# Optimization experiments

Measured on AMD Instinct MI355X. Metric: run time of the kernel, lower is better.

## Reference

```python
import jax, jax.numpy as jnp
import numpy as np

N = 100000
E = 3200000
NEG_SLOPE = 0.2  # PyG GATConv default


def gat_layer(x, src, dst, W, a_src, a_dst, b, heads, out_ch, concat):
    # per-node linear transform, split into heads: [N, H, C]
    h = (x @ W).reshape(N, heads, out_ch)
    # per-node attention logits: [N, H]
    al_src = jnp.sum(h * a_src, axis=-1)
    al_dst = jnp.sum(h * a_dst, axis=-1)
    # per-edge attention coefficient (x_j = source, x_i = target): [E, H]
    e = jax.nn.leaky_relu(al_src[src] + al_dst[dst], NEG_SLOPE)
    # segment softmax over incoming edges of each destination node
    m = jax.ops.segment_max(e, dst, num_segments=N)
    e = jnp.exp(e - m[dst])
    denom = jax.ops.segment_sum(e, dst, num_segments=N)
    alpha = e / (denom[dst] + 1e-16)
    # weighted message aggregation: scatter-add over dst
    msg = h[src] * alpha[..., None]  # [E, H, C]
    out = jax.ops.segment_sum(msg, dst, num_segments=N)  # [N, H, C]
    out = out.reshape(N, heads * out_ch) if concat else out.mean(axis=1)
    return out + b


def setup_inputs() -> dict:
    key = jax.random.key(0)
    ks = jax.random.split(key, 11)
    return {
        "x": jax.random.normal(ks[0], (N, 2), dtype=jnp.float32),
        "edge_index": jax.random.randint(ks[1], (2, E), 0, N, dtype=jnp.int64),
        "edge_attr": jax.random.normal(ks[2], (E, 1), dtype=jnp.float32),
        "W1": jax.random.normal(ks[3], (2, 32), dtype=jnp.float32) * 0.5,
        "att_src1": jax.random.normal(ks[4], (4, 8), dtype=jnp.float32) * 0.3,
        "att_dst1": jax.random.normal(ks[5], (4, 8), dtype=jnp.float32) * 0.3,
        "b1": jnp.zeros((32,), dtype=jnp.float32),
        "W2": jax.random.normal(ks[6], (32, 2), dtype=jnp.float32) * 0.2,
        "att_src2": jax.random.normal(ks[7], (1, 2), dtype=jnp.float32) * 0.3,
        "att_dst2": jax.random.normal(ks[8], (1, 2), dtype=jnp.float32) * 0.3,
        "b2": jnp.zeros((2,), dtype=jnp.float32),
    }


def reference(x, edge_index, edge_attr, W1, att_src1, att_dst1, b1, W2, att_src2, att_dst2, b2):
    # add self-loops (PyG GATConv default add_self_loops=True)
    loops = jnp.arange(N, dtype=edge_index.dtype)
    src = jnp.concatenate([edge_index[0], loops])
    dst = jnp.concatenate([edge_index[1], loops])
    h = gat_layer(x, src, dst, W1, att_src1, att_dst1, b1, heads=4, out_ch=8, concat=True)
    h = jax.nn.elu(h)
    out = gat_layer(h, src, dst, W2, att_src2, att_dst2, b2, heads=1, out_ch=2, concat=False)
    return out
```

## Files before the change

kernel.cpp:

```cpp
#include <hip/hip_runtime.h>
#include <math.h>

#define NEG_SLOPE 0.2f
#define BK_BITS 8
#define BK (1 << BK_BITS)
#define SBITS 17
#define SMASK ((1 << SBITS) - 1)
#define CAP 9216
#define CELL 80
#define NSLOT (256 * CELL)
#define RNDS 20
#define SW(p) ((p) ^ (((p) >> 5) & 31))

__device__ __forceinline__ float lrelu(float x) { return x > 0.f ? x : NEG_SLOPE * x; }

__global__ __launch_bounds__(1024) void bucket_scatter(const int* __restrict__ src,
                                                       const int* __restrict__ dst,
                                                       int* __restrict__ cnt_g,
                                                       int* __restrict__ cells, int E) {
    __shared__ int cnt[512], off[512], cur[512];
    __shared__ int2 lpair[12504];
    __shared__ int sTot;
    int t = threadIdx.x;
    int blk = blockIdx.x;
    int nb = gridDim.x;
    if (t < 512) cnt[t] = 0;
    __syncthreads();

    int E4 = E >> 2;
    int chunk4 = (E4 + nb - 1) / nb;
    const int4* src4 = (const int4*)src;
    const int4* dst4 = (const int4*)dst;
    int base4 = blk * chunk4;
    int4 d4[4], s4[4];
    bool val[4];
#pragma unroll
    for (int k = 0; k < 4; k++) {
        int o = k * 1024 + t;
        int i4 = base4 + o;
        val[k] = (o < chunk4) && (i4 < E4);
        if (val[k]) { d4[k] = dst4[i4]; s4[k] = src4[i4]; }
    }
    int dt = -1, st = 0;
    if (blk == nb - 1) {
        int e = (E4 << 2) + t;
        if (e < E) { dt = dst[e]; st = src[e]; }
    }
#pragma unroll
    for (int k = 0; k < 4; k++) {
        if (val[k]) {
            atomicAdd(&cnt[d4[k].x >> BK_BITS], 1);
            atomicAdd(&cnt[d4[k].y >> BK_BITS], 1);
            atomicAdd(&cnt[d4[k].z >> BK_BITS], 1);
            atomicAdd(&cnt[d4[k].w >> BK_BITS], 1);
        }
    }
    if (dt >= 0) atomicAdd(&cnt[dt >> BK_BITS], 1);
    __syncthreads();

    if (t < 512) cnt_g[blk * 512 + t] = min(cnt[t], CELL);
    if (t < 64) {
        int v[8], mysum = 0;
#pragma unroll
        for (int k = 0; k < 8; k++) { v[k] = cnt[t * 8 + k]; mysum += v[k]; }
        int s = mysum;
#pragma unroll
        for (int o = 1; o < 64; o <<= 1) {
            int u = __shfl_up(s, o);
            if (t >= o) s += u;
        }
        int run = s - mysum;
#pragma unroll
        for (int k = 0; k < 8; k++) {
            int d2 = t * 8 + k;
            off[d2] = run; cur[d2] = run;
            run += v[k];
        }
        if (t == 63) sTot = s;
    }
    __syncthreads();
    int total = sTot;

#pragma unroll
    for (int k = 0; k < 4; k++) {
        if (val[k]) {
            int slot;
            slot = atomicAdd(&cur[d4[k].x >> BK_BITS], 1); lpair[slot] = make_int2(d4[k].x, s4[k].x);
            slot = atomicAdd(&cur[d4[k].y >> BK_BITS], 1); lpair[slot] = make_int2(d4[k].y, s4[k].y);
            slot = atomicAdd(&cur[d4[k].z >> BK_BITS], 1); lpair[slot] = make_int2(d4[k].z, s4[k].z);
            slot = atomicAdd(&cur[d4[k].w >> BK_BITS], 1); lpair[slot] = make_int2(d4[k].w, s4[k].w);
        }
    }
    if (dt >= 0) {
        int slot = atomicAdd(&cur[dt >> BK_BITS], 1);
        lpair[slot] = make_int2(dt, st);
    }
    __syncthreads();

    int cellbase = blk * CELL;
    for (int i = t; i < total; i += 1024) {
        int2 e = lpair[i];
        int b = e.x >> BK_BITS;
        int slot = i - off[b];
        if (slot < CELL)
            cells[(size_t)b * NSLOT + cellbase + slot] =
                ((e.x & (BK - 1)) << SBITS) | e.y;
    }
}

__global__ __launch_bounds__(1024) void agg1_sortgather(
        const int* __restrict__ cells, const int* __restrict__ cnt_g,
        const float2* __restrict__ x2,
        const float* __restrict__ W1, const float* __restrict__ asrc,
        const float* __restrict__ adst, const float* __restrict__ b1,
        const float* __restrict__ W2, const float* __restrict__ as2,
        const float* __restrict__ ad2,
        float2* __restrict__ h2, float* __restrict__ al2d,
        int* __restrict__ rowdeg, int* __restrict__ pairs2, int N) {
    __shared__ float sW[64], sB[32], sW2[64], sP[4], sQ[4], sPd[4], sQd[4], sA2[4];
    __shared__ int cnt[BK], off[BK], cur[BK];
    __shared__ int ccnt[256];
    __shared__ int sorted[CAP];
    int t = threadIdx.x;
    int b = blockIdx.x;
    if (t < 64) { sW[t] = W1[t]; sW2[t] = W2[t]; }
    if (t < 32) sB[t] = b1[t];
    if (t < 2) { sA2[t] = as2[t]; sA2[2 + t] = ad2[t]; }
    if (t >= 64 && t < 68) {
        int tt = t - 64;
        float P = 0.f, Q = 0.f, Pd = 0.f, Qd = 0.f;
#pragma unroll
        for (int k = 0; k < 8; k++) {
            int c = tt * 8 + k;
            float a = asrc[c], ad_ = adst[c];
            float w0 = W1[c], w1 = W1[32 + c];
            P += w0 * a; Q += w1 * a;
            Pd += w0 * ad_; Qd += w1 * ad_;
        }
        sP[tt] = P; sQ[tt] = Q; sPd[tt] = Pd; sQd[tt] = Qd;
    }
    if (t >= 256 && t < 512) ccnt[t - 256] = cnt_g[(t - 256) * 512 + b];
    if (t >= 512 && t < 512 + BK) cnt[t - 512] = 0;
    __syncthreads();

    int dbase = b << BK_BITS;
    int ndst = min(BK, N - dbase);
    size_t base = (size_t)b * NSLOT;

    int myp[RNDS];
#pragma unroll
    for (int r = 0; r < RNDS; r++) {
        int s = t + r * 1024;
        int cb = s / CELL;
        bool v = (s - cb * CELL) < ccnt[cb];
        myp[r] = v ? cells[base + s] : -1;
    }
#pragma unroll
    for (int r = 0; r < RNDS; r++) {
        if (myp[r] >= 0) atomicAdd(&cnt[myp[r] >> SBITS], 1);
    }
    __syncthreads();

    if (t < 64) {
        int v[4], mysum = 0;
#pragma unroll
        for (int k = 0; k < 4; k++) { v[k] = cnt[t * 4 + k]; mysum += v[k]; }
        int s = mysum;
#pragma unroll
        for (int o = 1; o < 64; o <<= 1) {
            int u = __shfl_up(s, o);
            if (t >= o) s += u;
        }
        int run = s - mysum;
#pragma unroll
        for (int k = 0; k < 4; k++) {
            int d2 = t * 4 + k;
            off[d2] = run; cur[d2] = run;
            run += v[k];
        }
    }
    __syncthreads();

#pragma unroll
    for (int r = 0; r < RNDS; r++) {
        int p = myp[r];
        if (p >= 0) {
            int pos = atomicAdd(&cur[p >> SBITS], 1);
            sorted[SW(pos)] = p & SMASK;
        }
    }
    __syncthreads();

    for (int i = t; i < CAP; i += 1024) pairs2[b * CAP + i] = sorted[SW(i)];
    if (t < ndst) rowdeg[dbase + t] = (off[t] << 8) | min(cnt[t], 255);

    int d = t >> 2, q = t & 3;
    if (d < ndst) {
        int n = dbase + d;
        float rP[4], rQ[4], ald[4];
        float2 xd = x2[n];
#pragma unroll
        for (int h = 0; h < 4; h++) {
            rP[h] = sP[h]; rQ[h] = sQ[h];
            ald[h] = xd.x * sPd[h] + xd.y * sQd[h];
        }
        int deg = cnt[d];
        int start = off[d];
        int ids[16];
#pragma unroll
        for (int k = 0; k < 16; k++) {
            int j = q + 4 * k;
            ids[k] = (j < deg) ? sorted[SW(start + j)] : -1;
        }
        float Sw[4] = {0.f, 0.f, 0.f, 0.f};
        float S0[4] = {0.f, 0.f, 0.f, 0.f};
        float S1[4] = {0.f, 0.f, 0.f, 0.f};
#pragma unroll
        for (int half = 0; half < 2; half++) {
            float2 xv[8];
#pragma unroll
            for (int k = 0; k < 8; k++) {
                int id = ids[half * 8 + k];
                xv[k] = x2[id >= 0 ? id : 0];
            }
#pragma unroll
            for (int k = 0; k < 8; k++) {
                if (ids[half * 8 + k] >= 0) {
#pragma unroll
                    for (int h = 0; h < 4; h++) {
                        float e = lrelu(fmaf(xv[k].x, rP[h], fmaf(xv[k].y, rQ[h], ald[h])));
                        float w = __expf(fminf(e, 80.f));
                        Sw[h] += w; S0[h] += w * xv[k].x; S1[h] += w * xv[k].y;
                    }
                }
            }
        }
        for (int j = q + 64; j < deg; j += 4) {
            int s = sorted[SW(start + j)];
            float2 xs = x2[s];
#pragma unroll
            for (int h = 0; h < 4; h++) {
                float e = lrelu(fmaf(xs.x, rP[h], fmaf(xs.y, rQ[h], ald[h])));
                float w = __expf(fminf(e, 80.f));
                Sw[h] += w; S0[h] += w * xs.x; S1[h] += w * xs.y;
            }
        }
#pragma unroll
        for (int o = 1; o <= 2; o <<= 1) {
#pragma unroll
            for (int h = 0; h < 4; h++) {
                Sw[h] += __shfl_xor(Sw[h], o);
                S0[h] += __shfl_xor(S0[h], o);
                S1[h] += __shfl_xor(S1[h], o);
            }
        }
        if (q == 0) {
#pragma unroll
            for (int h = 0; h < 4; h++) {
                float e = lrelu(fmaf(xd.x, rP[h], fmaf(xd.y, rQ[h], ald[h])));
                float w = __expf(fminf(e, 80.f));
                Sw[h] += w; S0[h] += w * xd.x; S1[h] += w * xd.y;
            }
            float r[4];
#pragma unroll
            for (int h = 0; h < 4; h++) r[h] = 1.f / (Sw[h] + 1e-16f);
            float h20 = 0.f, h21 = 0.f;
#pragma unroll
            for (int c = 0; c < 32; c++) {
                int h = c >> 3;
                float outc = (sW[c] * S0[h] + sW[32 + c] * S1[h]) * r[h];
                float v2 = outc + sB[c];
                v2 = v2 > 0.f ? v2 : __expf(v2) - 1.f;
                h20 = fmaf(v2, sW2[2 * c], h20);
                h21 = fmaf(v2, sW2[2 * c + 1], h21);
            }
            h2[n] = make_float2(h20, h21);
            al2d[n] = h20 * sA2[2] + h21 * sA2[3];
        }
    }
}

__global__ __launch_bounds__(1024) void agg2_gather(
        const int* __restrict__ pairs2, const int* __restrict__ rowdeg,
        const float2* __restrict__ h2, const float* __restrict__ al2d,
        const float* __restrict__ as2, const float* __restrict__ b2,
        float2* __restrict__ out, int N) {
    int t = threadIdx.x;
    int b = blockIdx.x;
    int dbase = b << BK_BITS;
    int ndst = min(BK, N - dbase);
    int d = t >> 2, q = t & 3;
    if (d >= ndst) return;
    float a0 = as2[0], a1 = as2[1];

    int n = dbase + d;
    int rd = rowdeg[n];
    int start = rd >> 8;
    int deg = rd & 255;
    const int* lst = pairs2 + b * CAP + start;
    float ald = al2d[n];
    float2 hd = h2[n];
    int ids[16];
#pragma unroll
    for (int k = 0; k < 16; k++) {
        int j = q + 4 * k;
        ids[k] = (j < deg) ? lst[j] : -1;
    }
    float wsum = 0.f, ax = 0.f, ay = 0.f;
#pragma unroll
    for (int half = 0; half < 2; half++) {
        float2 hv[8];
#pragma unroll
        for (int k = 0; k < 8; k++) {
            int id = ids[half * 8 + k];
            hv[k] = h2[id >= 0 ? id : 0];
        }
#pragma unroll
        for (int k = 0; k < 8; k++) {
            if (ids[half * 8 + k] >= 0) {
                float e = lrelu(fmaf(hv[k].x, a0, fmaf(hv[k].y, a1, ald)));
                float w = __expf(fminf(e, 80.f));
                wsum += w; ax = fmaf(w, hv[k].x, ax); ay = fmaf(w, hv[k].y, ay);
            }
        }
    }
    for (int j = q + 64; j < deg; j += 4) {
        int s = lst[j];
        float2 hv = h2[s];
        float e = lrelu(fmaf(hv.x, a0, fmaf(hv.y, a1, ald)));
        float w = __expf(fminf(e, 80.f));
        wsum += w; ax = fmaf(w, hv.x, ax); ay = fmaf(w, hv.y, ay);
    }
#pragma unroll
    for (int o = 1; o <= 2; o <<= 1) {
        wsum += __shfl_xor(wsum, o);
        ax += __shfl_xor(ax, o);
        ay += __shfl_xor(ay, o);
    }
    if (q == 0) {
        float e = lrelu(fmaf(hd.x, a0, fmaf(hd.y, a1, ald)));
        float w = __expf(fminf(e, 80.f));
        wsum += w; ax = fmaf(w, hd.x, ax); ay = fmaf(w, hd.y, ay);
        float inv = 1.f / (wsum + 1e-16f);
        out[n] = make_float2(ax * inv + b2[0], ay * inv + b2[1]);
    }
}

extern "C" void kernel_launch(void* const* d_in, const int* in_sizes, int n_in,
                              void* d_out, int out_size, void* d_ws, size_t ws_size,
                              hipStream_t stream) {
    const float* x     = (const float*)d_in[0];
    const int*   eidx  = (const int*)d_in[1];
    const float* W1    = (const float*)d_in[3];
    const float* asrc1 = (const float*)d_in[4];
    const float* adst1 = (const float*)d_in[5];
    const float* b1    = (const float*)d_in[6];
    const float* W2    = (const float*)d_in[7];
    const float* asrc2 = (const float*)d_in[8];
    const float* adst2 = (const float*)d_in[9];
    const float* b2    = (const float*)d_in[10];

    const int N = in_sizes[0] / 2;
    const int E = in_sizes[1] / 2;
    const int* src = eidx;
    const int* dst = eidx + E;
    const int NB = (N + BK - 1) >> BK_BITS;
    const int nblk = 256;

    float* w = (float*)d_ws;
    float2* h2    = (float2*)w;
    float*  al2d  = w + 2 * (size_t)N;
    int* ip       = (int*)(w + 3 * (size_t)N);
    int* rowdeg   = ip;
    int* cnt_g    = ip + (size_t)N;
    int* pairs2   = cnt_g + (size_t)nblk * 512;
    int* cells    = pairs2 + (size_t)NB * CAP;

    bucket_scatter<<<nblk, 1024, 0, stream>>>(src, dst, cnt_g, cells, E);
    agg1_sortgather<<<NB, 1024, 0, stream>>>(cells, cnt_g, (const float2*)x,
                                             W1, asrc1, adst1, b1, W2, asrc2, adst2,
                                             h2, al2d, rowdeg, pairs2, N);
    agg2_gather<<<NB, 1024, 0, stream>>>(pairs2, rowdeg, (const float2*)h2, al2d,
                                         asrc2, b2, (float2*)d_out, N);
}
```

Baseline: 155.2 us.

## Replace fixed per-block cells with atomic-offset compact bucket arrays; split epilogue across lanes

The bucket scatter now reserves contiguous space in each destination bucket through a global atomic counter, so the pairs land compacted in a CAP-sized region per bucket. This replaces the padded 256x80 cell layout, so the aggregation kernel reads about 9 entries per thread instead of 20 padded slots and no longer needs the per-block count table. It adds a memset launch and global atomics, and edge order within a bucket becomes nondeterministic. Separately, the layer-1 epilogue (self-loop term, 32-channel ELU and projection) is spread across the 4 lanes per node, each handling one head, then combined with shuffles instead of running on lane 0 alone.

```diff
diff --git a/kernel.cpp b/kernel.cpp
--- a/kernel.cpp
+++ b/kernel.cpp
@@ -7,18 +7,17 @@
 #define SBITS 17
 #define SMASK ((1 << SBITS) - 1)
 #define CAP 9216
-#define CELL 80
-#define NSLOT (256 * CELL)
-#define RNDS 20
+#define PPT1 9
 #define SW(p) ((p) ^ (((p) >> 5) & 31))
+#define BCUR(b) ((b) * 16)
 
 __device__ __forceinline__ float lrelu(float x) { return x > 0.f ? x : NEG_SLOPE * x; }
 
 __global__ __launch_bounds__(1024) void bucket_scatter(const int* __restrict__ src,
                                                        const int* __restrict__ dst,
-                                                       int* __restrict__ cnt_g,
-                                                       int* __restrict__ cells, int E) {
-    __shared__ int cnt[512], off[512], cur[512];
+                                                       int* __restrict__ bcur,
+                                                       int* __restrict__ pairs, int E) {
+    __shared__ int cnt[512], off[512], cur[512], adj[512];
     __shared__ int2 lpair[12504];
     __shared__ int sTot;
     int t = threadIdx.x;
@@ -58,7 +57,6 @@
     if (dt >= 0) atomicAdd(&cnt[dt >> BK_BITS], 1);
     __syncthreads();
 
-    if (t < 512) cnt_g[blk * 512 + t] = min(cnt[t], CELL);
     if (t < 64) {
         int v[8], mysum = 0;
 #pragma unroll
@@ -77,6 +75,11 @@
             run += v[k];
         }
         if (t == 63) sTot = s;
+    }
+    __syncthreads();
+    if (t < 512 && cnt[t] > 0) {
+        int g0 = atomicAdd(&bcur[BCUR(t)], cnt[t]);
+        adj[t] = t * CAP + g0 - off[t];
     }
     __syncthreads();
     int total = sTot;
@@ -97,19 +100,17 @@
     }
     __syncthreads();
 
-    int cellbase = blk * CELL;
     for (int i = t; i < total; i += 1024) {
         int2 e = lpair[i];
         int b = e.x >> BK_BITS;
-        int slot = i - off[b];
-        if (slot < CELL)
-            cells[(size_t)b * NSLOT + cellbase + slot] =
-                ((e.x & (BK - 1)) << SBITS) | e.y;
+        int pos = adj[b] + i;
+        if (pos - b * CAP < CAP)
+            pairs[pos] = ((e.x & (BK - 1)) << SBITS) | e.y;
     }
 }
 
 __global__ __launch_bounds__(1024) void agg1_sortgather(
-        const int* __restrict__ cells, const int* __restrict__ cnt_g,
+        const int* __restrict__ pairs, const int* __restrict__ bcur,
         const float2* __restrict__ x2,
         const float* __restrict__ W1, const float* __restrict__ asrc,
         const float* __restrict__ adst, const float* __restrict__ b1,
@@ -119,7 +120,6 @@
         int* __restrict__ rowdeg, int* __restrict__ pairs2, int N) {
     __shared__ float sW[64], sB[32], sW2[64], sP[4], sQ[4], sPd[4], sQd[4], sA2[4];
     __shared__ int cnt[BK], off[BK], cur[BK];
-    __shared__ int ccnt[256];
     __shared__ int sorted[CAP];
     int t = threadIdx.x;
     int b = blockIdx.x;
@@ -139,25 +139,23 @@
         }
         sP[tt] = P; sQ[tt] = Q; sPd[tt] = Pd; sQd[tt] = Qd;
     }
-    if (t >= 256 && t < 512) ccnt[t - 256] = cnt_g[(t - 256) * 512 + b];
     if (t >= 512 && t < 512 + BK) cnt[t - 512] = 0;
     __syncthreads();
 
     int dbase = b << BK_BITS;
     int ndst = min(BK, N - dbase);
-    size_t base = (size_t)b * NSLOT;
-
-    int myp[RNDS];
-#pragma unroll
-    for (int r = 0; r < RNDS; r++) {
-        int s = t + r * 1024;
-        int cb = s / CELL;
-        bool v = (s - cb * CELL) < ccnt[cb];
-        myp[r] = v ? cells[base + s] : -1;
-    }
-#pragma unroll
-    for (int r = 0; r < RNDS; r++) {
-        if (myp[r] >= 0) atomicAdd(&cnt[myp[r] >> SBITS], 1);
+    int lo = b * CAP;
+    int hi = lo + min(bcur[BCUR(b)], CAP);
+
+    int myp[PPT1];
+#pragma unroll
+    for (int k = 0; k < PPT1; k++) {
+        int i = lo + t + k * 1024;
+        myp[k] = (i < hi) ? pairs[i] : -1;
+    }
+#pragma unroll
+    for (int k = 0; k < PPT1; k++) {
+        if (myp[k] >= 0) atomicAdd(&cnt[myp[k] >> SBITS], 1);
     }
     __syncthreads();
 
@@ -182,8 +180,8 @@
     __syncthreads();
 
 #pragma unroll
-    for (int r = 0; r < RNDS; r++) {
-        int p = myp[r];
+    for (int k = 0; k < PPT1; k++) {
+        int p = myp[k];
         if (p >= 0) {
             int pos = atomicAdd(&cur[p >> SBITS], 1);
             sorted[SW(pos)] = p & SMASK;
@@ -254,26 +252,30 @@
                 S1[h] += __shfl_xor(S1[h], o);
             }
         }
+#pragma unroll
+        for (int h = 0; h < 4; h++) {
+            float e = lrelu(fmaf(xd.x, rP[h], fmaf(xd.y, rQ[h], ald[h])));
+            float w = __expf(fminf(e, 80.f));
+            Sw[h] += w; S0[h] += w * xd.x; S1[h] += w * xd.y;
+        }
+        float rq = 1.f / (Sw[q] + 1e-16f);
+        float s0q = S0[q], s1q = S1[q];
+        float h20 = 0.f, h21 = 0.f;
+#pragma unroll
+        for (int k = 0; k < 8; k++) {
+            int c = q * 8 + k;
+            float outc = (sW[c] * s0q + sW[32 + c] * s1q) * rq;
+            float v2 = outc + sB[c];
+            v2 = v2 > 0.f ? v2 : __expf(v2) - 1.f;
+            h20 = fmaf(v2, sW2[2 * c], h20);
+            h21 = fmaf(v2, sW2[2 * c + 1], h21);
+        }
+#pragma unroll
+        for (int o = 1; o <= 2; o <<= 1) {
+            h20 += __shfl_xor(h20, o);
+            h21 += __shfl_xor(h21, o);
+        }
         if (q == 0) {
-#pragma unroll
-            for (int h = 0; h < 4; h++) {
-                float e = lrelu(fmaf(xd.x, rP[h], fmaf(xd.y, rQ[h], ald[h])));
-                float w = __expf(fminf(e, 80.f));
-                Sw[h] += w; S0[h] += w * xd.x; S1[h] += w * xd.y;
-            }
-            float r[4];
-#pragma unroll
-            for (int h = 0; h < 4; h++) r[h] = 1.f / (Sw[h] + 1e-16f);
-            float h20 = 0.f, h21 = 0.f;
-#pragma unroll
-            for (int c = 0; c < 32; c++) {
-                int h = c >> 3;
-                float outc = (sW[c] * S0[h] + sW[32 + c] * S1[h]) * r[h];
-                float v2 = outc + sB[c];
-                v2 = v2 > 0.f ? v2 : __expf(v2) - 1.f;
-                h20 = fmaf(v2, sW2[2 * c], h20);
-                h21 = fmaf(v2, sW2[2 * c + 1], h21);
-            }
             h2[n] = make_float2(h20, h21);
             al2d[n] = h20 * sA2[2] + h21 * sA2[3];
         }
@@ -372,12 +374,13 @@
     float*  al2d  = w + 2 * (size_t)N;
     int* ip       = (int*)(w + 3 * (size_t)N);
     int* rowdeg   = ip;
-    int* cnt_g    = ip + (size_t)N;
-    int* pairs2   = cnt_g + (size_t)nblk * 512;
-    int* cells    = pairs2 + (size_t)NB * CAP;
-
-    bucket_scatter<<<nblk, 1024, 0, stream>>>(src, dst, cnt_g, cells, E);
-    agg1_sortgather<<<NB, 1024, 0, stream>>>(cells, cnt_g, (const float2*)x,
+    int* bcur     = ip + (size_t)N;
+    int* pairs    = bcur + 8192;
+    int* pairs2   = pairs + (size_t)NB * CAP;
+
+    hipMemsetAsync(bcur, 0, 8192 * sizeof(int), stream);
+    bucket_scatter<<<nblk, 1024, 0, stream>>>(src, dst, bcur, pairs, E);
+    agg1_sortgather<<<NB, 1024, 0, stream>>>(pairs, bcur, (const float2*)x,
                                              W1, asrc1, adst1, b1, W2, asrc2, adst2,
                                              h2, al2d, rowdeg, pairs2, N);
     agg2_gather<<<NB, 1024, 0, stream>>>(pairs2, rowdeg, (const float2*)h2, al2d,
```

New measurement: 157.0 us. About the same (+1.1%).
